# Optimization experiments

Hardware: AMD Instinct MI355X
Metric: run time of the kernel (lower is better)

The kernel has to match this reference:

```python
import jax, jax.numpy as jnp
import numpy as np

HEADS = 16
CHANNELS = 1024
CPH = CHANNELS // HEADS
B, S = 2, 2048


def setup_inputs() -> dict:
    key = jax.random.key(0)
    ks = jax.random.split(key, 10)
    scale = 1.0 / np.sqrt(CHANNELS)
    inp = {
        "Q": jax.random.normal(ks[0], (B, CHANNELS, S), dtype=jnp.float32),
        "K": jax.random.normal(ks[1], (B, CHANNELS, S), dtype=jnp.float32),
        "V": jax.random.normal(ks[2], (B, CHANNELS, S), dtype=jnp.float32),
        "mask": jax.random.randint(ks[3], (B, S, S), 0, 2).astype(bool),
        # nn.Linear params: weight [out, in], bias [out]
        "Wq": jax.random.uniform(ks[4], (CHANNELS, CHANNELS), jnp.float32, -scale, scale),
        "bq": jax.random.uniform(ks[5], (CHANNELS,), jnp.float32, -scale, scale),
        "Wk": jax.random.uniform(ks[6], (CHANNELS, CHANNELS), jnp.float32, -scale, scale),
        "bk": jax.random.uniform(ks[7], (CHANNELS,), jnp.float32, -scale, scale),
        "Wv": jax.random.uniform(ks[8], (CHANNELS, CHANNELS), jnp.float32, -scale, scale),
        "bv": jax.random.uniform(ks[9], (CHANNELS,), jnp.float32, -scale, scale),
    }
    return inp


def reference(Q, K, V, mask, Wq, bq, Wk, bk, Wv, bv):
    b = Q.shape[0]
    # inputs are [B, C, S] -> transpose to [B, S, C], project, split heads
    def proj(x, W, bias):
        y = jnp.einsum('bcs,oc->bso', x, W) + bias  # [B, S, C]
        return y.reshape(b, -1, HEADS, CPH).transpose(0, 2, 1, 3)  # [B, H, S, cph]

    q = proj(Q, Wq, bq)
    k = proj(K, Wk, bk)
    v = proj(V, Wv, bv)
    scores = jnp.einsum('bhqd,bhkd->bhqk', q, k) / np.sqrt(CPH).astype(np.float32)
    scores = jnp.where(mask[:, None, :, :], jnp.float32(-1e9), scores)
    attn = jax.nn.softmax(scores, axis=-1)
    ctx = jnp.einsum('bhqk,bhkd->bhqd', attn, v)  # [B, H, S, cph]
    return ctx.transpose(0, 2, 1, 3).reshape(b, -1, HEADS * CPH)
```

## Files before the change

kernel.cpp:

```cpp
#include <hip/hip_runtime.h>
#include <hip/hip_bf16.h>
#include <stdint.h>

#define NH   16
#define CPH  64
#define CH   1024
#define BATCH 2
#define SEQ  2048

typedef __bf16    bf16x8 __attribute__((ext_vector_type(8)));
typedef float     f32x4  __attribute__((ext_vector_type(4)));
typedef uint16_t  u16x8  __attribute__((ext_vector_type(8)));

static __device__ inline uint16_t f2bf(float f) {
  union { float f; unsigned u; } v; v.f = f;
  unsigned r = (v.u + 0x7FFFu + ((v.u >> 16) & 1u)) >> 16;
  return (uint16_t)r;
}

static __device__ inline float fast_exp2(float x) {
  float r;
  asm("v_exp_f32 %0, %1" : "=v"(r) : "v"(x));
  return r;
}

__global__ void k_packmask(const void* __restrict__ mask,
                           unsigned long long* __restrict__ pm) {
  int row  = blockIdx.x * 4 + (threadIdx.x >> 6);
  int lane = threadIdx.x & 63;
  unsigned probe = ((const unsigned*)mask)[lane];
  bool imode = (__ballot(probe <= 1u) == ~0ull);
  unsigned long long* prow = pm + (size_t)row * (SEQ / 64);
  if (imode) {
    const int* m = (const int*)mask + (size_t)row * SEQ;
    for (int wi = 0; wi < SEQ / 64; wi++) {
      unsigned long long bits = __ballot(m[wi * 64 + lane] != 0);
      if (lane == 0) prow[wi] = bits;
    }
  } else {
    const unsigned char* m = (const unsigned char*)mask + (size_t)row * SEQ;
    for (int wi = 0; wi < SEQ / 64; wi++) {
      unsigned long long bits = __ballot(m[wi * 64 + lane] != 0);
      if (lane == 0) prow[wi] = bits;
    }
  }
}

__global__ void k_castw(const float* __restrict__ W0, const float* __restrict__ W1,
                        const float* __restrict__ W2, uint16_t* __restrict__ dst) {
  const float* W = blockIdx.z == 0 ? W0 : (blockIdx.z == 1 ? W1 : W2);
  uint16_t* o = dst + (size_t)blockIdx.z * (CH * CH);
  int idx = (blockIdx.x * 256 + threadIdx.x) * 4;
  float4 w = *(const float4*)(W + idx);
  o[idx + 0] = f2bf(w.x); o[idx + 1] = f2bf(w.y);
  o[idx + 2] = f2bf(w.z); o[idx + 3] = f2bf(w.w);
}

__global__ void k_transpose(const float* __restrict__ Q, const float* __restrict__ K,
                            const float* __restrict__ V, uint16_t* __restrict__ XT) {
  int z = blockIdx.z;
  int p = z % 3, b = z / 3;
  const float* X = (p == 0 ? Q : (p == 1 ? K : V)) + (size_t)b * CH * SEQ;
  uint16_t* T = XT + ((size_t)p * BATCH + b) * SEQ * CH;
  __shared__ float t[32][33];
  int tx = threadIdx.x, ty = threadIdx.y;
  int s0 = blockIdx.x * 32, c0 = blockIdx.y * 32;
#pragma unroll
  for (int i = 0; i < 4; i++)
    t[ty + 8 * i][tx] = X[(size_t)(c0 + ty + 8 * i) * SEQ + s0 + tx];
  __syncthreads();
  int tid2 = ty * 32 + tx;
  int c2 = tid2 & 15, sl = tid2 >> 4;
#pragma unroll
  for (int j = 0; j < 2; j++) {
    int s = sl + 16 * j;
    unsigned pk = (unsigned)f2bf(t[c2 * 2][s]) |
                  ((unsigned)f2bf(t[c2 * 2 + 1][s]) << 16);
    *(unsigned*)&T[(size_t)(s0 + s) * CH + c0 + c2 * 2] = pk;
  }
}

__global__ __launch_bounds__(256)
void k_proj(const uint16_t* __restrict__ XT, const uint16_t* __restrict__ Wbf,
            const float* __restrict__ bq, const float* __restrict__ bk,
            const float* __restrict__ bv,
            uint16_t* __restrict__ qbuf, uint16_t* __restrict__ kbuf,
            uint16_t* __restrict__ vtbuf) {
  int z = blockIdx.z, p = z % 3, b = z / 3;
  const uint16_t* X = XT + ((size_t)p * BATCH + b) * SEQ * CH;
  const uint16_t* W = Wbf + (size_t)p * CH * CH;
  const float* bias = p == 0 ? bq : (p == 1 ? bk : bv);
  int s0 = blockIdx.x * 128, o0 = blockIdx.y * 128;

  __shared__ __align__(16) uint16_t Al[128 * 64];
  __shared__ __align__(16) uint16_t Bl[128 * 64];

  int tid = threadIdx.x, lane = tid & 63, w = tid >> 6;
  int g = lane >> 4, li = lane & 15;
  int wm = w >> 1, wn = w & 1;
  int lr = lane >> 3, lc = lane & 7;

  f32x4 acc[4][4] = {};

  for (int c0 = 0; c0 < CH; c0 += 64) {
    const uint16_t* gA = W + (size_t)(o0 + w * 32) * CH + c0;
    const uint16_t* gB = X + (size_t)(s0 + w * 32) * CH + c0;
#pragma unroll
    for (int i = 0; i < 4; i++) {
      __builtin_amdgcn_global_load_lds(
          (const __attribute__((address_space(1))) void*)(gA + (size_t)(i * 8 + lr) * CH + lc * 8),
          (__attribute__((address_space(3))) void*)(Al + (w * 32 + i * 8) * 64),
          16, 0, 0);
      __builtin_amdgcn_global_load_lds(
          (const __attribute__((address_space(1))) void*)(gB + (size_t)(i * 8 + lr) * CH + lc * 8),
          (__attribute__((address_space(3))) void*)(Bl + (w * 32 + i * 8) * 64),
          16, 0, 0);
    }
    __syncthreads();

#pragma unroll
    for (int ks = 0; ks < 2; ks++) {
      bf16x8 af[4], bfr[4];
#pragma unroll
      for (int mt = 0; mt < 4; mt++)
        af[mt] = *(const bf16x8*)&Al[(wm * 64 + mt * 16 + li) * 64 + ks * 32 + g * 8];
#pragma unroll
      for (int nt = 0; nt < 4; nt++)
        bfr[nt] = *(const bf16x8*)&Bl[(wn * 64 + nt * 16 + li) * 64 + ks * 32 + g * 8];
#pragma unroll
      for (int mt = 0; mt < 4; mt++)
#pragma unroll
        for (int nt = 0; nt < 4; nt++)
          acc[mt][nt] = __builtin_amdgcn_mfma_f32_16x16x32_bf16(af[mt], bfr[nt], acc[mt][nt], 0, 0, 0);
    }
    __syncthreads();
  }

  int h = (o0 >> 6) + wm;
  float scale = (p == 0) ? 0.18033688011112042f : 1.0f;
  size_t bh = (size_t)b * NH + h;
#pragma unroll
  for (int mt = 0; mt < 4; mt++) {
#pragma unroll
    for (int r = 0; r < 4; r++) {
      int dd = mt * 16 + g * 4 + r;
      float bi = bias[o0 + wm * 64 + dd];
#pragma unroll
      for (int nt = 0; nt < 4; nt++) {
        int s = s0 + wn * 64 + nt * 16 + li;
        float v = (acc[mt][nt][r] + bi) * scale;
        if (p == 2)
          vtbuf[(bh * CPH + dd) * SEQ + s] = f2bf(v);
        else {
          uint16_t* dst = (p == 0) ? qbuf : kbuf;
          dst[(bh * SEQ + s) * CPH + dd] = f2bf(v);
        }
      }
    }
  }
}

__global__ __launch_bounds__(256, 4)
void k_attn(const uint16_t* __restrict__ qbuf, const uint16_t* __restrict__ kbuf,
            const uint16_t* __restrict__ vtbuf,
            const unsigned long long* __restrict__ pm, float* __restrict__ out) {
  int bid = blockIdx.x;
  int logical = (bid & 7) * 128 + (bid >> 3);
  int bx = logical & 31, bhh = logical >> 5;
  int b = bhh >> 4, h = bhh & 15;
  int q0 = bx * 64;
  const uint16_t* qb = qbuf + ((size_t)b * NH + h) * SEQ * CPH;
  const uint16_t* kb = kbuf + ((size_t)b * NH + h) * SEQ * CPH;
  const uint16_t* vt = vtbuf + ((size_t)b * NH + h) * CPH * SEQ;
  const unsigned long long* pmb = pm + (size_t)b * SEQ * (SEQ / 64);
  int tid = threadIdx.x, lane = tid & 63, w = tid >> 6;
  int g = lane >> 4, li = lane & 15;
  int qw = q0 + w * 16;
  __shared__ uint16_t Kl[64][80];
  __shared__ uint16_t Vl[64][80];
  __shared__ uint16_t Pl[4][16][76];

  bf16x8 aq[2];
#pragma unroll
  for (int ks = 0; ks < 2; ks++)
    aq[ks] = *(const bf16x8*)&qb[(size_t)(qw + li) * CPH + ks * 32 + g * 8];

  u16x8 oneu = {0x3F80, 0x3F80, 0x3F80, 0x3F80, 0x3F80, 0x3F80, 0x3F80, 0x3F80};
  bf16x8 ones = *(bf16x8*)&oneu;

  f32x4 octx[4] = {{0,0,0,0},{0,0,0,0},{0,0,0,0},{0,0,0,0}};
  f32x4 sacc = {0,0,0,0};

  int r8 = tid >> 3, ch = tid & 7;

  for (int kv0 = 0; kv0 < SEQ; kv0 += 64) {
    int kw = kv0 >> 6;
#pragma unroll
    for (int i = 0; i < 64; i += 32) {
      *(u16x8*)&Kl[r8 + i][ch * 8] =
          *(const u16x8*)&kb[(size_t)(kv0 + r8 + i) * CPH + ch * 8];
      *(u16x8*)&Vl[r8 + i][ch * 8] =
          *(const u16x8*)&vt[(size_t)(r8 + i) * SEQ + kv0 + ch * 8];
    }
    unsigned long long mw[4];
#pragma unroll
    for (int r = 0; r < 4; r++)
      mw[r] = pmb[(size_t)(qw + g * 4 + r) * (SEQ / 64) + kw];
    __syncthreads();

    f32x4 sc[4] = {{0,0,0,0},{0,0,0,0},{0,0,0,0},{0,0,0,0}};
#pragma unroll
    for (int ks = 0; ks < 2; ks++)
#pragma unroll
      for (int nt = 0; nt < 4; nt++) {
        bf16x8 kf = *(const bf16x8*)&Kl[nt * 16 + li][ks * 32 + g * 8];
        sc[nt] = __builtin_amdgcn_mfma_f32_16x16x32_bf16(aq[ks], kf, sc[nt], 0, 0, 0);
      }

#pragma unroll
    for (int nt = 0; nt < 4; nt++)
#pragma unroll
      for (int r = 0; r < 4; r++) {
        float e = fast_exp2(sc[nt][r]);
        unsigned bit = (unsigned)(mw[r] >> (nt * 16 + li)) & 1u;
        float pv = bit ? 0.0f : e;
        Pl[w][g * 4 + r][nt * 16 + li] = f2bf(pv);
      }

#pragma unroll
    for (int ks = 0; ks < 2; ks++) {
      bf16x8 ap = *(const bf16x8*)&Pl[w][li][ks * 32 + g * 8];
      sacc = __builtin_amdgcn_mfma_f32_16x16x32_bf16(ap, ones, sacc, 0, 0, 0);
#pragma unroll
      for (int nt = 0; nt < 4; nt++) {
        bf16x8 vf = *(const bf16x8*)&Vl[nt * 16 + li][ks * 32 + g * 8];
        octx[nt] = __builtin_amdgcn_mfma_f32_16x16x32_bf16(ap, vf, octx[nt], 0, 0, 0);
      }
    }
    __syncthreads();
  }

#pragma unroll
  for (int r = 0; r < 4; r++) {
    float inv = 1.0f / sacc[r];
    int qrow = qw + g * 4 + r;
#pragma unroll
    for (int nt = 0; nt < 4; nt++) {
      int d = nt * 16 + li;
      out[((size_t)b * SEQ + qrow) * CH + h * CPH + d] = octx[nt][r] * inv;
    }
  }
}

extern "C" void kernel_launch(void* const* d_in, const int* in_sizes, int n_in,
                              void* d_out, int out_size, void* d_ws, size_t ws_size,
                              hipStream_t stream) {
  (void)in_sizes; (void)n_in; (void)out_size; (void)ws_size;
  const float* Q  = (const float*)d_in[0];
  const float* K  = (const float*)d_in[1];
  const float* V  = (const float*)d_in[2];
  const void*  Mk = d_in[3];
  const float* Wq = (const float*)d_in[4];
  const float* bq = (const float*)d_in[5];
  const float* Wk = (const float*)d_in[6];
  const float* bk = (const float*)d_in[7];
  const float* Wv = (const float*)d_in[8];
  const float* bv = (const float*)d_in[9];
  char* ws = (char*)d_ws;

  uint16_t* XT    = (uint16_t*)(ws + 256);
  uint16_t* Wbf   = (uint16_t*)(ws + 256 + 3ull * BATCH * SEQ * CH * 2);
  uint16_t* qbuf  = (uint16_t*)((char*)Wbf + 3ull * CH * CH * 2);
  uint16_t* kbuf  = qbuf + (size_t)BATCH * NH * SEQ * CPH;
  uint16_t* vtbuf = kbuf + (size_t)BATCH * NH * SEQ * CPH;
  unsigned long long* pmask = (unsigned long long*)XT;
  float* out = (float*)d_out;

  hipLaunchKernelGGL(k_castw, dim3(CH * CH / 1024, 1, 3), dim3(256), 0, stream,
                     Wq, Wk, Wv, Wbf);
  hipLaunchKernelGGL(k_transpose, dim3(SEQ / 32, CH / 32, 6), dim3(32, 8), 0, stream,
                     Q, K, V, XT);
  hipLaunchKernelGGL(k_proj, dim3(SEQ / 128, CH / 128, 6), dim3(256), 0, stream,
                     XT, Wbf, bq, bk, bv, qbuf, kbuf, vtbuf);
  hipLaunchKernelGGL(k_packmask, dim3(BATCH * SEQ / 4), dim3(256), 0, stream,
                     Mk, pmask);
  hipLaunchKernelGGL(k_attn, dim3(1024), dim3(256), 0, stream,
                     qbuf, kbuf, vtbuf, pmask, out);
}
```

Baseline: 153.5 us.

## Merge weight cast, transpose and mask packing into one prep kernel; remap proj blocks

```diff
diff --git a/kernel.cpp b/kernel.cpp
--- a/kernel.cpp
+++ b/kernel.cpp
@@ -24,59 +24,69 @@
   return r;
 }
 
-__global__ void k_packmask(const void* __restrict__ mask,
-                           unsigned long long* __restrict__ pm) {
-  int row  = blockIdx.x * 4 + (threadIdx.x >> 6);
-  int lane = threadIdx.x & 63;
-  unsigned probe = ((const unsigned*)mask)[lane];
+__global__ __launch_bounds__(256)
+void k_prep(const float* __restrict__ Q, const float* __restrict__ K,
+            const float* __restrict__ V, const void* __restrict__ Mk,
+            const float* __restrict__ W0, const float* __restrict__ W1,
+            const float* __restrict__ W2,
+            uint16_t* __restrict__ Wbf, uint16_t* __restrict__ XT,
+            unsigned long long* __restrict__ pm) {
+  int bb = blockIdx.x;
+  int tid = threadIdx.x;
+
+  if (bb < 3072) {
+    int wz = bb >> 10, bx = bb & 1023;
+    const float* W = wz == 0 ? W0 : (wz == 1 ? W1 : W2);
+    uint16_t* o = Wbf + (size_t)wz * (CH * CH);
+    int idx = (bx * 256 + tid) * 4;
+    float4 w = *(const float4*)(W + idx);
+    o[idx + 0] = f2bf(w.x); o[idx + 1] = f2bf(w.y);
+    o[idx + 2] = f2bf(w.z); o[idx + 3] = f2bf(w.w);
+    return;
+  }
+
+  if (bb < 15360) {
+    int t3 = bb - 3072;
+    int x = t3 & 63, y = (t3 >> 6) & 31, z = t3 >> 11;
+    int p = z % 3, b = z / 3;
+    const float* X = (p == 0 ? Q : (p == 1 ? K : V)) + (size_t)b * CH * SEQ;
+    uint16_t* T = XT + ((size_t)p * BATCH + b) * SEQ * CH;
+    __shared__ float t[32][33];
+    int tx = tid & 31, ty = tid >> 5;
+    int s0 = x * 32, c0 = y * 32;
+#pragma unroll
+    for (int i = 0; i < 4; i++)
+      t[ty + 8 * i][tx] = X[(size_t)(c0 + ty + 8 * i) * SEQ + s0 + tx];
+    __syncthreads();
+    int c2 = tid & 15, sl = tid >> 4;
+#pragma unroll
+    for (int j = 0; j < 2; j++) {
+      int s = sl + 16 * j;
+      unsigned pk = (unsigned)f2bf(t[c2 * 2][s]) |
+                    ((unsigned)f2bf(t[c2 * 2 + 1][s]) << 16);
+      *(unsigned*)&T[(size_t)(s0 + s) * CH + c0 + c2 * 2] = pk;
+    }
+    return;
+  }
+
+  int pb = bb - 15360;
+  int row  = pb * 4 + (tid >> 6);
+  int lane = tid & 63;
+  unsigned probe = ((const unsigned*)Mk)[lane];
   bool imode = (__ballot(probe <= 1u) == ~0ull);
   unsigned long long* prow = pm + (size_t)row * (SEQ / 64);
   if (imode) {
-    const int* m = (const int*)mask + (size_t)row * SEQ;
+    const int* m = (const int*)Mk + (size_t)row * SEQ;
     for (int wi = 0; wi < SEQ / 64; wi++) {
       unsigned long long bits = __ballot(m[wi * 64 + lane] != 0);
       if (lane == 0) prow[wi] = bits;
     }
   } else {
-    const unsigned char* m = (const unsigned char*)mask + (size_t)row * SEQ;
+    const unsigned char* m = (const unsigned char*)Mk + (size_t)row * SEQ;
     for (int wi = 0; wi < SEQ / 64; wi++) {
       unsigned long long bits = __ballot(m[wi * 64 + lane] != 0);
       if (lane == 0) prow[wi] = bits;
     }
-  }
-}
-
-__global__ void k_castw(const float* __restrict__ W0, const float* __restrict__ W1,
-                        const float* __restrict__ W2, uint16_t* __restrict__ dst) {
-  const float* W = blockIdx.z == 0 ? W0 : (blockIdx.z == 1 ? W1 : W2);
-  uint16_t* o = dst + (size_t)blockIdx.z * (CH * CH);
-  int idx = (blockIdx.x * 256 + threadIdx.x) * 4;
-  float4 w = *(const float4*)(W + idx);
-  o[idx + 0] = f2bf(w.x); o[idx + 1] = f2bf(w.y);
-  o[idx + 2] = f2bf(w.z); o[idx + 3] = f2bf(w.w);
-}
-
-__global__ void k_transpose(const float* __restrict__ Q, const float* __restrict__ K,
-                            const float* __restrict__ V, uint16_t* __restrict__ XT) {
-  int z = blockIdx.z;
-  int p = z % 3, b = z / 3;
-  const float* X = (p == 0 ? Q : (p == 1 ? K : V)) + (size_t)b * CH * SEQ;
-  uint16_t* T = XT + ((size_t)p * BATCH + b) * SEQ * CH;
-  __shared__ float t[32][33];
-  int tx = threadIdx.x, ty = threadIdx.y;
-  int s0 = blockIdx.x * 32, c0 = blockIdx.y * 32;
-#pragma unroll
-  for (int i = 0; i < 4; i++)
-    t[ty + 8 * i][tx] = X[(size_t)(c0 + ty + 8 * i) * SEQ + s0 + tx];
-  __syncthreads();
-  int tid2 = ty * 32 + tx;
-  int c2 = tid2 & 15, sl = tid2 >> 4;
-#pragma unroll
-  for (int j = 0; j < 2; j++) {
-    int s = sl + 16 * j;
-    unsigned pk = (unsigned)f2bf(t[c2 * 2][s]) |
-                  ((unsigned)f2bf(t[c2 * 2 + 1][s]) << 16);
-    *(unsigned*)&T[(size_t)(s0 + s) * CH + c0 + c2 * 2] = pk;
   }
 }
 
@@ -86,11 +96,14 @@
             const float* __restrict__ bv,
             uint16_t* __restrict__ qbuf, uint16_t* __restrict__ kbuf,
             uint16_t* __restrict__ vtbuf) {
-  int z = blockIdx.z, p = z % 3, b = z / 3;
+  int bid = blockIdx.x;
+  int l = (bid & 7) * 96 + (bid >> 3);
+  int sx = l & 15, tt = l >> 4, oy = tt & 7, z = tt >> 3;
+  int p = z % 3, b = z / 3;
   const uint16_t* X = XT + ((size_t)p * BATCH + b) * SEQ * CH;
   const uint16_t* W = Wbf + (size_t)p * CH * CH;
   const float* bias = p == 0 ? bq : (p == 1 ? bk : bv);
-  int s0 = blockIdx.x * 128, o0 = blockIdx.y * 128;
+  int s0 = sx * 128, o0 = oy * 128;
 
   __shared__ __align__(16) uint16_t Al[128 * 64];
   __shared__ __align__(16) uint16_t Bl[128 * 64];
@@ -273,17 +286,13 @@
   uint16_t* qbuf  = (uint16_t*)((char*)Wbf + 3ull * CH * CH * 2);
   uint16_t* kbuf  = qbuf + (size_t)BATCH * NH * SEQ * CPH;
   uint16_t* vtbuf = kbuf + (size_t)BATCH * NH * SEQ * CPH;
-  unsigned long long* pmask = (unsigned long long*)XT;
+  unsigned long long* pmask = (unsigned long long*)((char*)vtbuf + (size_t)BATCH * NH * SEQ * CPH * 2);
   float* out = (float*)d_out;
 
-  hipLaunchKernelGGL(k_castw, dim3(CH * CH / 1024, 1, 3), dim3(256), 0, stream,
-                     Wq, Wk, Wv, Wbf);
-  hipLaunchKernelGGL(k_transpose, dim3(SEQ / 32, CH / 32, 6), dim3(32, 8), 0, stream,
-                     Q, K, V, XT);
-  hipLaunchKernelGGL(k_proj, dim3(SEQ / 128, CH / 128, 6), dim3(256), 0, stream,
+  hipLaunchKernelGGL(k_prep, dim3(16384), dim3(256), 0, stream,
+                     Q, K, V, Mk, Wq, Wk, Wv, Wbf, XT, pmask);
+  hipLaunchKernelGGL(k_proj, dim3(768), dim3(256), 0, stream,
                      XT, Wbf, bq, bk, bv, qbuf, kbuf, vtbuf);
-  hipLaunchKernelGGL(k_packmask, dim3(BATCH * SEQ / 4), dim3(256), 0, stream,
-                     Mk, pmask);
   hipLaunchKernelGGL(k_attn, dim3(1024), dim3(256), 0, stream,
                      qbuf, kbuf, vtbuf, pmask, out);
 }
```

Result: no change. 151.2 us (-1.5%).
